# Performance work log

Hardware: AMD Instinct MI355X
Metric: run time of the kernel (lower is better)

Reference implementation:

```python
import jax, jax.numpy as jnp
import numpy as np

B, N, E = 8, 4096, 524288
BN = B * N


def setup_inputs() -> dict:
    key = jax.random.key(0)
    ks = jax.random.split(key, 24)
    def w(k, shape):
        return jax.random.normal(k, shape, dtype=jnp.float32) * 0.05
    return {
        "x": jax.random.normal(ks[0], (B, 3, N), dtype=jnp.float32),
        "emb": jax.random.normal(ks[1], (B, 32, N), dtype=jnp.float32),
        "edge_index": jax.random.randint(ks[2], (2, E), 0, BN),
        "e": 0,
        "g_w": w(ks[3], (3, 64)),   "g_b": jnp.zeros((64,), jnp.float32),
        "c_w": w(ks[4], (32, 64)),  "c_b": jnp.zeros((64,), jnp.float32),
        "m1_w1": w(ks[5], (64, 128)),  "m1_b1": jnp.zeros((128,), jnp.float32),
        "m1_w2": w(ks[6], (128, 128)), "m1_b2": jnp.zeros((128,), jnp.float32),
        "m2_w1": w(ks[7], (128, 128)), "m2_b1": jnp.zeros((128,), jnp.float32),
        "m2_w2": w(ks[8], (128, 256)), "m2_b2": jnp.zeros((256,), jnp.float32),
        "m3_w1": w(ks[9], (512, 512)), "m3_b1": jnp.zeros((512,), jnp.float32),
        "m3_w2": w(ks[10], (512, 1024)), "m3_b2": jnp.zeros((1024,), jnp.float32),
        "fc_w": w(ks[11], (64, 256)), "fc_b": jnp.zeros((256,), jnp.float32),
    }


def reference(x, emb, edge_index, e,
              g_w, g_b, c_w, c_b,
              m1_w1, m1_b1, m1_w2, m1_b2,
              m2_w1, m2_b1, m2_w2, m2_b2,
              m3_w1, m3_b1, m3_w2, m3_b2,
              fc_w, fc_b):
    # Conv1d with kernel_size=1 == per-point linear: [B,Cin,N] -> [B,Cout,N]
    xg = jax.nn.relu(jnp.einsum('bcn,cd->bdn', x, g_w) + g_b[None, :, None])
    ce = jax.nn.relu(jnp.einsum('bcn,cd->bdn', emb, c_w) + c_b[None, :, None])
    feat = ce if e == 1 else xg                       # [B,64,N]
    f = feat.transpose(0, 2, 1).reshape(-1, 64)        # [B*N,64]

    src, tgt = edge_index[0], edge_index[1]

    def gin(h, w1, b1, w2, b2):
        # GINConv (eps=0): mlp(h + sum_{j->i} h_j)
        agg = jax.ops.segment_sum(h[src], tgt, num_segments=BN)
        z = h + agg
        return jax.nn.relu(z @ w1 + b1) @ w2 + b2

    f1 = jax.nn.relu(gin(f, m1_w1, m1_b1, m1_w2, m1_b2))    # [B*N,128]
    f2 = jax.nn.relu(gin(f1, m2_w1, m2_b1, m2_w2, m2_b2))   # [B*N,256]
    feat1 = f1.reshape(B, N, 128).transpose(0, 2, 1)        # [B,128,N]
    feat2 = f2.reshape(B, N, 256).transpose(0, 2, 1)        # [B,256,N]

    oth_in = xg if e == 1 else ce                           # other modality
    oth = jax.nn.relu(jnp.einsum('bcn,cd->bnd', oth_in, fc_w) + fc_b)  # [B,N,256]
    oth = oth.transpose(0, 2, 1)                            # [B,256,N]

    fused = jnp.concatenate([feat2, oth], axis=1)           # [B,512,N]
    ff = fused.transpose(0, 2, 1).reshape(-1, 512)          # [B*N,512]
    f3 = gin(ff, m3_w1, m3_b1, m3_w2, m3_b2)                # [B*N,1024]
    feat3 = f3.reshape(B, N, 1024).transpose(0, 2, 1)       # [B,1024,N]

    return jnp.concatenate([feat1, feat2, feat3], axis=1)   # [B,1408,N]
```

## Files before the change

kernel.cpp:

```cpp
#include <hip/hip_runtime.h>

#define BN_   32768
#define NN    4096
#define EDGES 524288
#define DEGCAP 64

typedef __attribute__((ext_vector_type(8))) __bf16 bf16x8;
typedef __attribute__((ext_vector_type(4))) float f32x4;

__global__ void build_adj(const int* __restrict__ src, const int* __restrict__ tgt,
                          int* __restrict__ cnt, int* __restrict__ adj){
  int i = blockIdx.x*256 + threadIdx.x;
  if (i < EDGES){
    int t = tgt[i];
    int pos = atomicAdd(&cnt[t], 1);
    if (pos < DEGCAP) adj[(size_t)t*DEGCAP + pos] = src[i];
  }
}

__global__ void wtrans_all(const float* __restrict__ w11, const float* __restrict__ w12,
                           const float* __restrict__ w21, const float* __restrict__ w22,
                           const float* __restrict__ w31, const float* __restrict__ w32,
                           __bf16* o11, __bf16* o12, __bf16* o21, __bf16* o22,
                           __bf16* o31, __bf16* o32)
{
  int idx = blockIdx.x*256 + threadIdx.x;
  const float* src; __bf16* d; int N, K, base;
  if (idx < 8192)        { src=w11; d=o11; K=64;  N=128;  base=0; }
  else if (idx < 24576)  { src=w12; d=o12; K=128; N=128;  base=8192; }
  else if (idx < 40960)  { src=w21; d=o21; K=128; N=128;  base=24576; }
  else if (idx < 73728)  { src=w22; d=o22; K=128; N=256;  base=40960; }
  else if (idx < 335872) { src=w31; d=o31; K=512; N=512;  base=73728; }
  else if (idx < 860160) { src=w32; d=o32; K=512; N=1024; base=335872; }
  else return;
  int t = idx - base;
  int k = t / N, n = t - k*N;
  d[(size_t)n*K + k] = (__bf16)src[t];
}

__global__ __launch_bounds__(256)
void conv_kernel(const float* __restrict__ x, const float* __restrict__ emb,
                 const int* __restrict__ eflag,
                 const float* __restrict__ g_w, const float* __restrict__ g_b,
                 const float* __restrict__ c_w, const float* __restrict__ c_b,
                 const float* __restrict__ fc_w, const float* __restrict__ fc_b,
                 __bf16* __restrict__ F0, __bf16* __restrict__ FF)
{
  __shared__ float xs[3][16];
  __shared__ float es[32][16];
  __shared__ float sel[16][64];
  const int tid = threadIdx.x;
  const int node0 = blockIdx.x * 16;
  const int b  = node0 >> 12;
  const int nl = node0 & 4095;
  const int e  = *eflag;

  if (tid < 48){
    int c = tid >> 4, i = tid & 15;
    xs[c][i] = x[(size_t)b*3*NN + c*NN + nl + i];
  }
  {
    int idx = tid;
#pragma unroll
    for (int p=0;p<2;p++){
      int c = idx >> 4, i = idx & 15;
      es[c][i] = emb[(size_t)b*32*NN + c*NN + nl + i];
      idx += 256;
    }
  }
  __syncthreads();
  {
    const int ch = tid & 63;
    const int g  = tid >> 6;
    float gw[3], cw[32];
#pragma unroll
    for (int c=0;c<3;c++)  gw[c] = g_w[c*64 + ch];
#pragma unroll
    for (int c=0;c<32;c++) cw[c] = c_w[c*64 + ch];
    float gb = g_b[ch], cb = c_b[ch];
#pragma unroll
    for (int q=0;q<4;q++){
      int n = g*4 + q;
      float a = gb;
#pragma unroll
      for (int c=0;c<3;c++) a += xs[c][n]*gw[c];
      float xg = fmaxf(a, 0.f);
      float s2 = cb;
#pragma unroll
      for (int c=0;c<32;c++) s2 += es[c][n]*cw[c];
      float ce = fmaxf(s2, 0.f);
      float f0 = e ? ce : xg;
      float so = e ? xg : ce;
      F0[(size_t)(node0+n)*64 + ch] = (__bf16)f0;
      sel[n][ch] = so;
    }
  }
  __syncthreads();
  {
    const int h = tid;
    float acc[16];
#pragma unroll
    for (int i=0;i<16;i++) acc[i]=0.f;
    for (int k4=0;k4<16;k4++){
      float w0 = fc_w[(k4*4+0)*256 + h];
      float w1 = fc_w[(k4*4+1)*256 + h];
      float w2 = fc_w[(k4*4+2)*256 + h];
      float w3 = fc_w[(k4*4+3)*256 + h];
#pragma unroll
      for (int i=0;i<16;i++){
        float4 sv = *(const float4*)&sel[i][k4*4];
        acc[i] += sv.x*w0 + sv.y*w1 + sv.z*w2 + sv.w*w3;
      }
    }
    float fb = fc_b[h];
#pragma unroll
    for (int i=0;i<16;i++){
      float v = fmaxf(acc[i] + fb, 0.f);
      FF[(size_t)(node0+i)*512 + 256 + h] = (__bf16)v;
    }
  }
}

template<int C>
__global__ __launch_bounds__(256)
void gather_k(const __bf16* __restrict__ f, const int* __restrict__ cnt,
              const int* __restrict__ adj, __bf16* __restrict__ z)
{
  constexpr int TPN = C/8;
  const int tid  = threadIdx.x;
  int node = blockIdx.x*(256/TPN) + tid/TPN;
  if (TPN == 64) node = __builtin_amdgcn_readfirstlane(node);
  const int c8   = (tid & (TPN-1))*8;
  const int deg  = min(cnt[node], DEGCAP);
  const int* __restrict__ arow = adj + (size_t)node*DEGCAP;
  const __bf16* p = f + c8;
  float a[8];
  {
    bf16x8 sv = *(const bf16x8*)(p + (size_t)node*C);
#pragma unroll
    for (int t=0;t<8;t++) a[t] = (float)sv[t];
  }
  int j = 0;
  for (; j+8<=deg; j+=8){
    int sIdx[8];
#pragma unroll
    for (int u=0;u<8;u++) sIdx[u] = arow[j+u];
    bf16x8 v[8];
#pragma unroll
    for (int u=0;u<8;u++) v[u] = *(const bf16x8*)(p + (size_t)sIdx[u]*C);
#pragma unroll
    for (int u=0;u<8;u++)
#pragma unroll
      for (int t=0;t<8;t++) a[t] += (float)v[u][t];
  }
  for (; j+2<=deg; j+=2){
    int s0=arow[j], s1=arow[j+1];
    bf16x8 v0=*(const bf16x8*)(p+(size_t)s0*C), v1=*(const bf16x8*)(p+(size_t)s1*C);
#pragma unroll
    for (int t=0;t<8;t++) a[t] += (float)v0[t] + (float)v1[t];
  }
  if (j < deg){
    int s=arow[j];
    bf16x8 v=*(const bf16x8*)(p+(size_t)s*C);
#pragma unroll
    for (int t=0;t<8;t++) a[t] += (float)v[t];
  }
  bf16x8 o;
#pragma unroll
  for (int t=0;t<8;t++) o[t] = (__bf16)a[t];
  *(bf16x8*)(z + (size_t)node*C + c8) = o;
}

template<int K, int GSWAP>
__global__ __launch_bounds__(256, 2)
void mfma_gemm(const __bf16* __restrict__ A, const __bf16* __restrict__ B,
               const float* __restrict__ bias,
               __bf16* __restrict__ outr, int ostride,
               float* __restrict__ outT, int cbase, int relu)
{
  __shared__ __align__(16) char smem[17408];

  const int tid = threadIdx.x;
  const int l   = tid & 63;
  const int w   = tid >> 6;
  const int wm  = w >> 1, wn = w & 1;
  const int n0  = (GSWAP ? blockIdx.y : blockIdx.x) * 128;
  const int h0  = (GSWAP ? blockIdx.x : blockIdx.y) * 128;

  f32x4 acc[4][4];
#pragma unroll
  for (int m=0;m<4;m++)
#pragma unroll
    for (int n=0;n<4;n++) acc[m][n] = (f32x4){0.f,0.f,0.f,0.f};

  const __bf16* gsrc = (w<2) ? A : B;
  char* sdst = (w<2) ? smem : smem + 8192;
  const int rbase = (w<2) ? n0 : h0;
  const int ci0 = (w & 1) * 4;
  const int cd = (l&3) ^ ((l>>3)&3);
  const __bf16* g0 = gsrc + (size_t)(rbase + (l>>2))*K + cd*8;

  const int r16 = l & 15, q = l >> 4;
  const int fsw = ((q ^ ((r16>>1)&3)) << 4);

  for (int ks=0; ks<K/32; ks++){
    __syncthreads();
#pragma unroll
    for (int i=0;i<4;i++){
      __builtin_amdgcn_global_load_lds(
        (const __attribute__((address_space(1))) void*)(g0 + (size_t)(ci0+i)*16*K + ks*32),
        (__attribute__((address_space(3))) void*)(sdst + (ci0+i)*1024), 16, 0, 0);
    }
    __syncthreads();

    bf16x8 fa[4], fb[4];
#pragma unroll
    for (int m=0;m<4;m++){
      const int ro = (wm*64 + m*16 + r16)*64 + fsw;
      fa[m] = *(const bf16x8*)(smem + ro);
    }
#pragma unroll
    for (int n=0;n<4;n++){
      const int ro = (wn*64 + n*16 + r16)*64 + fsw;
      fb[n] = *(const bf16x8*)(smem + 8192 + ro);
    }
#pragma unroll
    for (int m=0;m<4;m++)
#pragma unroll
      for (int n=0;n<4;n++)
        acc[m][n] = __builtin_amdgcn_mfma_f32_16x16x32_bf16(fa[m], fb[n], acc[m][n], 0,0,0);
  }

  __syncthreads();
  float* scratch = (float*)(void*)smem + w*1088;

  float bv[4];
#pragma unroll
  for (int n=0;n<4;n++) bv[n] = bias[h0 + wn*64 + n*16 + r16];

#pragma unroll
  for (int m=0;m<4;m++){
#pragma unroll
    for (int n=0;n<4;n++)
#pragma unroll
      for (int r=0;r<4;r++){
        float v = acc[m][n][r] + bv[n];
        if (relu) v = fmaxf(v, 0.f);
        scratch[(q*4+r)*68 + n*16 + r16] = v;
      }
    if (outr){
      const int row = l>>2, ch = (l&3)*16;
      bf16x8 H0,H1;
#pragma unroll
      for (int t=0;t<16;t++){
        float x = scratch[row*68 + ch + t];
        if (t<8) H0[t]=(__bf16)x; else H1[t-8]=(__bf16)x;
      }
      size_t o = (size_t)(n0 + wm*64 + m*16 + row)*ostride + h0 + wn*64 + ch;
      *(bf16x8*)(outr+o)   = H0;
      *(bf16x8*)(outr+o+8) = H1;
    }
    if (outT){
      const int b = n0 >> 12, nl = n0 & 4095;
      const int rr0 = (l&3)*4;
#pragma unroll
      for (int j=0;j<4;j++){
        const int c = (l>>2) + 16*j;
        f32x4 v;
#pragma unroll
        for (int i=0;i<4;i++) v[i] = scratch[(rr0+i)*68 + c];
        size_t o = ((size_t)b*1408 + cbase + h0 + wn*64 + c)*NN + nl + wm*64 + m*16 + rr0;
        *(f32x4*)(outT + o) = v;
      }
    }
  }
}

extern "C" void kernel_launch(void* const* d_in, const int* in_sizes, int n_in,
                              void* d_out, int out_size, void* d_ws, size_t ws_size,
                              hipStream_t stream)
{
  const float* x     = (const float*)d_in[0];
  const float* emb   = (const float*)d_in[1];
  const int*   ei    = (const int*)d_in[2];
  const int*   eflag = (const int*)d_in[3];
  const float* g_w   = (const float*)d_in[4];
  const float* g_b   = (const float*)d_in[5];
  const float* c_w   = (const float*)d_in[6];
  const float* c_b   = (const float*)d_in[7];
  const float* m1w1  = (const float*)d_in[8];
  const float* m1b1  = (const float*)d_in[9];
  const float* m1w2  = (const float*)d_in[10];
  const float* m1b2  = (const float*)d_in[11];
  const float* m2w1  = (const float*)d_in[12];
  const float* m2b1  = (const float*)d_in[13];
  const float* m2w2  = (const float*)d_in[14];
  const float* m2b2  = (const float*)d_in[15];
  const float* m3w1  = (const float*)d_in[16];
  const float* m3b1  = (const float*)d_in[17];
  const float* m3w2  = (const float*)d_in[18];
  const float* m3b2  = (const float*)d_in[19];
  const float* fc_w  = (const float*)d_in[20];
  const float* fc_b  = (const float*)d_in[21];
  float* out = (float*)d_out;
  char*  ws  = (char*)d_ws;

  __bf16* F0 = (__bf16*)(ws + 0);
  __bf16* Z1 = (__bf16*)(ws + 4194304);
  __bf16* H1 = (__bf16*)(ws + 8388608);
  __bf16* F1 = (__bf16*)(ws + 16777216);
  __bf16* Z2 = (__bf16*)(ws + 25165824);
  __bf16* H2 = (__bf16*)(ws + 33554432);
  __bf16* FF = (__bf16*)(ws + 41943040);
  __bf16* Z3 = (__bf16*)(ws + 75497472);
  __bf16* H3 = (__bf16*)(ws + 109051904);
  char* wb = ws + 150994944;
  __bf16* W11=(__bf16*)(wb+0);
  __bf16* W12=(__bf16*)(wb+16384);
  __bf16* W21=(__bf16*)(wb+49152);
  __bf16* W22=(__bf16*)(wb+81920);
  __bf16* W31=(__bf16*)(wb+147456);
  __bf16* W32=(__bf16*)(wb+671744);
  int* adj = (int*)(ws + 153092096);
  int* cnt = (int*)(ws + 161480704);

  const int* srcp = ei;
  const int* tgtp = ei + EDGES;

  hipMemsetAsync(cnt, 0, BN_*4, stream);
  build_adj<<<EDGES/256, 256, 0, stream>>>(srcp, tgtp, cnt, adj);

  conv_kernel<<<BN_/16, 256, 0, stream>>>(x, emb, eflag, g_w, g_b, c_w, c_b,
                                          fc_w, fc_b, F0, FF);

  wtrans_all<<<3360, 256, 0, stream>>>(m1w1, m1w2, m2w1, m2w2, m3w1, m3w2,
                                       W11, W12, W21, W22, W31, W32);

  gather_k<64><<<BN_/32, 256, 0, stream>>>(F0, cnt, adj, Z1);
  mfma_gemm<64,0><<<dim3(BN_/128, 1), 256, 0, stream>>>(
      Z1, W11, m1b1, H1, 128, nullptr, 0, 1);
  mfma_gemm<128,0><<<dim3(BN_/128, 1), 256, 0, stream>>>(
      H1, W12, m1b2, F1, 128, out, 0, 1);

  gather_k<128><<<BN_/16, 256, 0, stream>>>(F1, cnt, adj, Z2);
  mfma_gemm<128,0><<<dim3(BN_/128, 1), 256, 0, stream>>>(
      Z2, W21, m2b1, H2, 128, nullptr, 0, 1);
  mfma_gemm<128,0><<<dim3(BN_/128, 2), 256, 0, stream>>>(
      H2, W22, m2b2, FF, 512, out, 128, 1);

  gather_k<512><<<BN_/4, 256, 0, stream>>>(FF, cnt, adj, Z3);
  mfma_gemm<512,1><<<dim3(4, BN_/128), 256, 0, stream>>>(
      Z3, W31, m3b1, H3, 512, nullptr, 0, 1);
  mfma_gemm<512,1><<<dim3(8, BN_/128), 256, 0, stream>>>(
      H3, W32, m3b2, nullptr, 0, out, 384, 0);
}
```

Measured before the change: 317.4 us.

## Double-buffer LDS tiles in MFMA GEMM to overlap global loads with compute

The GEMM main loop now uses two 16 KB shared-memory buffers and prefetches the next K-slice with global_load_lds while the current one feeds the MFMAs. It synchronises with explicit vmcnt waits and raw s_barrier instead of __syncthreads. It also raises wave priority around the MFMA block. LDS use grows from 17 KB to 32 KB per block, which could lower occupancy, and the hand-written waitcnt logic depends on the exact count of outstanding loads.

```diff
diff --git a/kernel.cpp b/kernel.cpp
--- a/kernel.cpp
+++ b/kernel.cpp
@@ -178,7 +178,8 @@
                __bf16* __restrict__ outr, int ostride,
                float* __restrict__ outT, int cbase, int relu)
 {
-  __shared__ __align__(16) char smem[17408];
+  constexpr int NK = K/32;
+  __shared__ __align__(16) char smem[32768];
 
   const int tid = threadIdx.x;
   const int l   = tid & 63;
@@ -194,7 +195,7 @@
     for (int n=0;n<4;n++) acc[m][n] = (f32x4){0.f,0.f,0.f,0.f};
 
   const __bf16* gsrc = (w<2) ? A : B;
-  char* sdst = (w<2) ? smem : smem + 8192;
+  const int soff = (w<2) ? 0 : 8192;
   const int rbase = (w<2) ? n0 : h0;
   const int ci0 = (w & 1) * 4;
   const int cd = (l&3) ^ ((l>>3)&3);
@@ -203,32 +204,51 @@
   const int r16 = l & 15, q = l >> 4;
   const int fsw = ((q ^ ((r16>>1)&3)) << 4);
 
-  for (int ks=0; ks<K/32; ks++){
-    __syncthreads();
+  auto STAGE = [&](int ks, int bb){
+    char* d = smem + bb*16384 + soff;
+    const __bf16* gk = g0 + ks*32;
 #pragma unroll
     for (int i=0;i<4;i++){
       __builtin_amdgcn_global_load_lds(
-        (const __attribute__((address_space(1))) void*)(g0 + (size_t)(ci0+i)*16*K + ks*32),
-        (__attribute__((address_space(3))) void*)(sdst + (ci0+i)*1024), 16, 0, 0);
-    }
-    __syncthreads();
-
+        (const __attribute__((address_space(1))) void*)(gk + (size_t)(ci0+i)*16*K),
+        (__attribute__((address_space(3))) void*)(d + (ci0+i)*1024), 16, 0, 0);
+    }
+  };
+
+  STAGE(0, 0);
+  STAGE(1, 1);
+
+  for (int ks=0; ks<NK; ks++){
+    const int bb = ks & 1;
+    if (ks < NK-1) asm volatile("s_waitcnt vmcnt(4)" ::: "memory");
+    else           asm volatile("s_waitcnt vmcnt(0)" ::: "memory");
+    asm volatile("s_barrier" ::: "memory");
+
+    const char* base = smem + bb*16384;
     bf16x8 fa[4], fb[4];
 #pragma unroll
     for (int m=0;m<4;m++){
       const int ro = (wm*64 + m*16 + r16)*64 + fsw;
-      fa[m] = *(const bf16x8*)(smem + ro);
+      fa[m] = *(const bf16x8*)(base + ro);
     }
 #pragma unroll
     for (int n=0;n<4;n++){
       const int ro = (wn*64 + n*16 + r16)*64 + fsw;
-      fb[n] = *(const bf16x8*)(smem + 8192 + ro);
-    }
+      fb[n] = *(const bf16x8*)(base + 8192 + ro);
+    }
+    asm volatile("s_waitcnt lgkmcnt(0)" ::: "memory");
+    __builtin_amdgcn_sched_barrier(0);
+
+    __builtin_amdgcn_s_setprio(1);
 #pragma unroll
     for (int m=0;m<4;m++)
 #pragma unroll
       for (int n=0;n<4;n++)
         acc[m][n] = __builtin_amdgcn_mfma_f32_16x16x32_bf16(fa[m], fb[n], acc[m][n], 0,0,0);
+    __builtin_amdgcn_s_setprio(0);
+
+    asm volatile("s_barrier" ::: "memory");
+    if (ks+2 < NK) STAGE(ks+2, bb);
   }
 
   __syncthreads();
```

Measured after the change: 311.2 us. About the same (-1.9%).
